# Performance work log

Hardware: AMD Instinct MI355X
Metric: run time of the kernel (lower is better)

Reference implementation:

```python
import jax, jax.numpy as jnp
import numpy as np

DIM_LIST = [8, 8, 8, 8, 8, 8, 8, 8]
RANK_LIST = [1, 64, 64, 64, 64, 64, 64, 64, 1]
ORDER = 4                      # tensor_input_order
PADDED_IN = int(np.prod(DIM_LIST[:ORDER]))   # 4096
NUM_OUT = int(np.prod(DIM_LIST[ORDER:]))     # 4096
BATCH = 8192
NUM_IN = 4000                  # < PADDED_IN, exercises padding path


def setup_inputs() -> dict:
    key = jax.random.key(0)
    keys = jax.random.split(key, 10)
    x = jax.random.normal(keys[0], (BATCH, NUM_IN), dtype=jnp.float32)
    cores = {}
    for i in range(8):
        shp = (RANK_LIST[i], DIM_LIST[i], RANK_LIST[i + 1])
        cores[f"c{i}"] = 0.1 * jax.random.normal(keys[1 + i], shp, dtype=jnp.float32)
    bias = jax.random.normal(keys[9], (NUM_OUT,), dtype=jnp.float32)
    return {"x": x, **cores, "bias": bias}


def _tt_forward(x, cores, bias):
    B = x.shape[0]
    pad = PADDED_IN - x.shape[-1]
    xp = jnp.pad(x, ((0, 0), (0, pad))) if pad > 0 else x
    # ---- contract input modes with first ORDER cores ----
    z = xp.reshape(B, DIM_LIST[0], -1)            # (B, d0, M)
    z = jnp.einsum('bdm,dr->bmr', z, cores[0][0])  # core0 has r0=1
    for i in range(1, ORDER):
        d = DIM_LIST[i]
        Bz, M, r = z.shape
        z = z.reshape(B, d, M // d, r)
        z = jnp.einsum('bdmr,rds->bms', z, cores[i])
    # z: (B, 1, r_k)
    y = z
    # ---- expand output modes with remaining cores ----
    for i in range(ORDER, len(DIM_LIST)):
        y = jnp.einsum('bpr,rds->bpds', y, cores[i])
        y = y.reshape(B, -1, cores[i].shape[-1])
    out = y.reshape(B, -1)[:, :NUM_OUT]
    return out + bias


def reference(x, c0, c1, c2, c3, c4, c5, c6, c7, bias):
    cores = [c0, c1, c2, c3, c4, c5, c6, c7]
    return _tt_forward(x, cores, bias)
```

## Files before the change

### kernel.cpp

```cpp
#include <hip/hip_runtime.h>
#include <hip/hip_bf16.h>


typedef __attribute__((ext_vector_type(8))) short short8;
typedef __attribute__((ext_vector_type(4))) short s16x4;
typedef __attribute__((ext_vector_type(4))) float f32x4;

__device__ __forceinline__ short f2bf(float f) {
    union { float f; unsigned u; } c; c.f = f;
    unsigned u = c.u;
    unsigned r = (u + 0x7fffu + ((u >> 16) & 1u)) >> 16;
    return (short)r;
}

__global__ __launch_bounds__(64) void tt_heads(
    const float* __restrict__ c0, const float* __restrict__ c1,
    const float* __restrict__ c6, const float* __restrict__ c7,
    float* __restrict__ A2, float* __restrict__ B6) {
    const int t = threadIdx.x;
    if (blockIdx.x < 64) {
        const int b = blockIdx.x, i = b >> 3, d = b & 7;
        float acc = 0.f;
        for (int r = 0; r < 64; ++r)
            acc += c0[i * 64 + r] * c1[(r * 8 + d) * 64 + t];
        A2[b * 64 + t] = acc;
    } else {
        const int r = blockIdx.x - 64, d = t >> 3, j = t & 7;
        float acc = 0.f;
        for (int q = 0; q < 64; ++q)
            acc += c6[(r * 8 + d) * 64 + q] * c7[q * 8 + j];
        B6[r * 64 + t] = acc;
    }
}

__global__ __launch_bounds__(64) void tt_seconds(
    const float* __restrict__ A2, const float* __restrict__ c2,
    const float* __restrict__ B6, const float* __restrict__ c5,
    float* __restrict__ A3, float* __restrict__ B5) {
    const int t = threadIdx.x;
    if (blockIdx.x < 512) {
        const int row = blockIdx.x, i = row >> 3, d = row & 7;
        float acc = 0.f;
        for (int r = 0; r < 64; ++r)
            acc += A2[i * 64 + r] * c2[(r * 8 + d) * 64 + t];
        A3[row * 64 + t] = acc;
    } else {
        const int bb = blockIdx.x - 512, r = bb >> 3, d = bb & 7;
        float acc = 0.f;
        for (int q = 0; q < 64; ++q)
            acc += c5[(r * 8 + d) * 64 + q] * B6[q * 64 + t];
        B5[r * 512 + d * 64 + t] = acc;
    }
}

__global__ __launch_bounds__(256) void tt_chain_wide(
    const float* __restrict__ A3, const float* __restrict__ c3,
    const float* __restrict__ B5, const float* __restrict__ c4,
    short* __restrict__ A4t, short* __restrict__ B4t) {
    const int bid = blockIdx.x, t = threadIdx.x;
    if (bid < 1024) {
        const int row = (bid << 2) | (t >> 6);
        const int s = t & 63;
        const int i = row >> 3, d = row & 7;
        float acc = 0.f;
        for (int r = 0; r < 64; ++r)
            acc += A3[i * 64 + r] * c3[(r * 8 + d) * 64 + s];
        A4t[s * 4096 + row] = f2bf(acc);
    } else {
        const int rd = bid - 1024;
        const int r = rd >> 3, d = rd & 7;
        for (int j = t; j < 512; j += 256) {
            float acc = 0.f;
            for (int q = 0; q < 64; ++q)
                acc += c4[(r * 8 + d) * 64 + q] * B5[q * 512 + j];
            B4t[(d * 512 + j) * 64 + r] = f2bf(acc);
        }
    }
}

__global__ __launch_bounds__(1024, 8) void gemm1_v2(
    const float* __restrict__ x, const short* __restrict__ A4t,
    short* __restrict__ zb) {
    __shared__ float zsm[16 * 1024];
    const int tid = threadIdx.x, wave = tid >> 6, lane = tid & 63;
    const int m0 = blockIdx.x << 4;
    const int r16 = lane & 15, hi = lane >> 4, kq = hi << 3;
    const float* xp = x + (long)(m0 + r16) * 4000 + kq;

    f32x4 acc[4] = {};
#pragma unroll 2
    for (int t = wave; t < 125; t += 16) {
        const int k0 = t << 5;
        f32x4 u0 = *(const f32x4*)(xp + k0);
        f32x4 u1 = *(const f32x4*)(xp + k0 + 4);
        short8 a;
        a[0] = f2bf(u0[0]); a[1] = f2bf(u0[1]);
        a[2] = f2bf(u0[2]); a[3] = f2bf(u0[3]);
        a[4] = f2bf(u1[0]); a[5] = f2bf(u1[1]);
        a[6] = f2bf(u1[2]); a[7] = f2bf(u1[3]);
#pragma unroll
        for (int f = 0; f < 4; ++f) {
            short8 b = *(const short8*)(A4t + (f * 16 + r16) * 4096 + k0 + kq);
            acc[f] = __builtin_amdgcn_mfma_f32_16x16x32_bf16(a, b, acc[f], 0, 0, 0);
        }
    }
    const int prow = hi << 2;
#pragma unroll
    for (int f = 0; f < 4; ++f)
#pragma unroll
        for (int u = 0; u < 4; ++u)
            zsm[wave * 1024 + (prow + u) * 64 + f * 16 + r16] = acc[f][u];
    __syncthreads();
    if (tid < 256) {
        const f32x4* zp = (const f32x4*)zsm;
        f32x4 s = zp[tid];
#pragma unroll
        for (int w = 1; w < 16; ++w) s += zp[w * 256 + tid];
        s16x4 o;
#pragma unroll
        for (int u = 0; u < 4; ++u) o[u] = f2bf(s[u]);
        const int orow = tid >> 4, ocol = (tid & 15) << 2;
        *(s16x4*)(zb + (m0 + orow) * 64 + ocol) = o;
    }
}

#define BM 128
#define BN 128
#define BK 32

template <int K>
__global__ __launch_bounds__(256) void gemm_bias_kernel(
    const short* __restrict__ A,
    const short* __restrict__ Bt,
    const float* __restrict__ bias,
    float* __restrict__ C) {
    constexpr int N = 4096;
    __shared__ short As[BM * BK];
    __shared__ short Bs[BN * BK];

    const int tid  = threadIdx.x;
    const int wave = tid >> 6;
    const int lane = tid & 63;

    const int bid = blockIdx.x;
    const int wg  = (bid & 7) * 256 + (bid >> 3);
    const int m0 = (wg >> 5) * BM;
    const int n0 = (wg & 31) * BN;

    const int c0i = tid;
    const int c1i = 256 + tid;
    const short* gA0 = A  + (m0 + (c0i >> 2)) * K + ((c0i & 3) << 3);
    const short* gA1 = A  + (m0 + (c1i >> 2)) * K + ((c1i & 3) << 3);
    const short* gB0 = Bt + (n0 + (c0i >> 2)) * K + ((c0i & 3) << 3);
    const short* gB1 = Bt + (n0 + (c1i >> 2)) * K + ((c1i & 3) << 3);
    short* lA0 = As + wave * 512;
    short* lA1 = As + 2048 + wave * 512;
    short* lB0 = Bs + wave * 512;
    short* lB1 = Bs + 2048 + wave * 512;

    const int wr = (wave >> 1) << 6;
    const int wc = (wave & 1) << 6;
    const int r16 = lane & 15;
    const int kq  = (lane >> 4) << 3;

    f32x4 acc[4][4] = {};

    for (int kt = 0; kt < K / BK; ++kt) {
        __builtin_amdgcn_global_load_lds((const __attribute__((address_space(1))) void*)gA0,
                                         (__attribute__((address_space(3))) void*)lA0, 16, 0, 0);
        __builtin_amdgcn_global_load_lds((const __attribute__((address_space(1))) void*)gA1,
                                         (__attribute__((address_space(3))) void*)lA1, 16, 0, 0);
        __builtin_amdgcn_global_load_lds((const __attribute__((address_space(1))) void*)gB0,
                                         (__attribute__((address_space(3))) void*)lB0, 16, 0, 0);
        __builtin_amdgcn_global_load_lds((const __attribute__((address_space(1))) void*)gB1,
                                         (__attribute__((address_space(3))) void*)lB1, 16, 0, 0);
        gA0 += BK; gA1 += BK; gB0 += BK; gB1 += BK;
        __syncthreads();

        short8 a[4], b[4];
#pragma unroll
        for (int f = 0; f < 4; ++f) {
            a[f] = *(const short8*)(As + (wr + f * 16 + r16) * BK + kq);
            b[f] = *(const short8*)(Bs + (wc + f * 16 + r16) * BK + kq);
        }
#pragma unroll
        for (int i = 0; i < 4; ++i)
#pragma unroll
            for (int j = 0; j < 4; ++j)
                acc[i][j] = __builtin_amdgcn_mfma_f32_16x16x32_bf16(
                    a[i], b[j], acc[i][j], 0, 0, 0);
        __syncthreads();
    }

    const int crow = m0 + wr + ((lane >> 4) << 2);
    const int ccol = n0 + wc + r16;
#pragma unroll
    for (int i = 0; i < 4; ++i) {
#pragma unroll
        for (int j = 0; j < 4; ++j) {
            const int r = crow + i * 16;
            const int c = ccol + j * 16;
            const float bz = bias[c];
#pragma unroll
            for (int u = 0; u < 4; ++u)
                C[(r + u) * N + c] = acc[i][j][u] + bz;
        }
    }
}

extern "C" void kernel_launch(void* const* d_in, const int* in_sizes, int n_in,
                              void* d_out, int out_size, void* d_ws, size_t ws_size,
                              hipStream_t stream) {
    const float* x    = (const float*)d_in[0];
    const float* c0   = (const float*)d_in[1];
    const float* c1   = (const float*)d_in[2];
    const float* c2   = (const float*)d_in[3];
    const float* c3   = (const float*)d_in[4];
    const float* c4   = (const float*)d_in[5];
    const float* c5   = (const float*)d_in[6];
    const float* c6   = (const float*)d_in[7];
    const float* c7   = (const float*)d_in[8];
    const float* bias = (const float*)d_in[9];
    float* out = (float*)d_out;

    char* ws = (char*)d_ws;
    short* zb  = (short*)ws;
    short* A4t = (short*)(ws + (1u << 20));
    short* B4t = (short*)(ws + (1u << 20) + (512u << 10));
    float* A2  = (float*)(ws + (2u << 20));
    float* A3  = A2 + 64 * 64;
    float* B6  = A3 + 512 * 64;
    float* B5  = B6 + 64 * 64;

    tt_heads<<<128, 64, 0, stream>>>(c0, c1, c6, c7, A2, B6);
    tt_seconds<<<1024, 64, 0, stream>>>(A2, c2, B6, c5, A3, B5);
    tt_chain_wide<<<1536, 256, 0, stream>>>(A3, c3, B5, c4, A4t, B4t);

    gemm1_v2<<<512, 1024, 0, stream>>>(x, A4t, zb);
    gemm_bias_kernel<64><<<2048, 256, 0, stream>>>(zb, B4t, bias, out);
}
```

Measured before the change: 96.09 us.

## Store A4 in MFMA fragment order and stage GEMM epilogue through LDS

The A4 factor is now written in a fragment-major layout, so each lane in gemm1 reads its 16-byte B operand from one contiguous 1 KB block per fragment instead of rows strided by 8 KB. The final GEMM's epilogue now goes through shared memory, reusing the operand buffers, so each thread writes full 16-byte float4 rows of the output with the bias added as a vector, replacing scattered scalar stores. This adds extra barriers and LDS traffic in the epilogue, and the producer kernel's writes become more scattered.

Result: faster. 81.62 us (-15.1%).

```diff
diff --git a/kernel.cpp b/kernel.cpp
--- a/kernel.cpp
+++ b/kernel.cpp
@@ -56,16 +56,17 @@
 __global__ __launch_bounds__(256) void tt_chain_wide(
     const float* __restrict__ A3, const float* __restrict__ c3,
     const float* __restrict__ B5, const float* __restrict__ c4,
-    short* __restrict__ A4t, short* __restrict__ B4t) {
+    short* __restrict__ A4f, short* __restrict__ B4t) {
     const int bid = blockIdx.x, t = threadIdx.x;
     if (bid < 1024) {
-        const int row = (bid << 2) | (t >> 6);
+        const int k = (bid << 2) | (t >> 6);
         const int s = t & 63;
-        const int i = row >> 3, d = row & 7;
+        const int i = k >> 3, d = k & 7;
         float acc = 0.f;
         for (int r = 0; r < 64; ++r)
             acc += A3[i * 64 + r] * c3[(r * 8 + d) * 64 + s];
-        A4t[s * 4096 + row] = f2bf(acc);
+        A4f[(((k >> 5) * 4 + (s >> 4)) << 9) + (((k >> 3) & 3) << 7) +
+            ((s & 15) << 3) + (k & 7)] = f2bf(acc);
     } else {
         const int rd = bid - 1024;
         const int r = rd >> 3, d = rd & 7;
@@ -79,13 +80,14 @@
 }
 
 __global__ __launch_bounds__(1024, 8) void gemm1_v2(
-    const float* __restrict__ x, const short* __restrict__ A4t,
+    const float* __restrict__ x, const short* __restrict__ A4f,
     short* __restrict__ zb) {
     __shared__ float zsm[16 * 1024];
     const int tid = threadIdx.x, wave = tid >> 6, lane = tid & 63;
     const int m0 = blockIdx.x << 4;
     const int r16 = lane & 15, hi = lane >> 4, kq = hi << 3;
     const float* xp = x + (long)(m0 + r16) * 4000 + kq;
+    const short* a4p = A4f + (lane << 3);
 
     f32x4 acc[4] = {};
 #pragma unroll 2
@@ -100,7 +102,7 @@
         a[6] = f2bf(u1[2]); a[7] = f2bf(u1[3]);
 #pragma unroll
         for (int f = 0; f < 4; ++f) {
-            short8 b = *(const short8*)(A4t + (f * 16 + r16) * 4096 + k0 + kq);
+            short8 b = *(const short8*)(a4p + (((t << 2) + f) << 9));
             acc[f] = __builtin_amdgcn_mfma_f32_16x16x32_bf16(a, b, acc[f], 0, 0, 0);
         }
     }
@@ -135,8 +137,10 @@
     const float* __restrict__ bias,
     float* __restrict__ C) {
     constexpr int N = 4096;
-    __shared__ short As[BM * BK];
-    __shared__ short Bs[BN * BK];
+    __shared__ __align__(16) char smem[16384];
+    short* As = (short*)smem;
+    short* Bs = (short*)(smem + 8192);
+    float* eps = (float*)smem;
 
     const int tid  = threadIdx.x;
     const int wave = tid >> 6;
@@ -161,7 +165,8 @@
     const int wr = (wave >> 1) << 6;
     const int wc = (wave & 1) << 6;
     const int r16 = lane & 15;
-    const int kq  = (lane >> 4) << 3;
+    const int hi  = lane >> 4;
+    const int kq  = hi << 3;
 
     f32x4 acc[4][4] = {};
 
@@ -192,18 +197,24 @@
         __syncthreads();
     }
 
-    const int crow = m0 + wr + ((lane >> 4) << 2);
-    const int ccol = n0 + wc + r16;
+    float* slab = eps + wave * 1024;
+    const f32x4 bzv = *(const f32x4*)(bias + n0 + wc + (r16 << 2));
 #pragma unroll
     for (int i = 0; i < 4; ++i) {
-#pragma unroll
-        for (int j = 0; j < 4; ++j) {
-            const int r = crow + i * 16;
-            const int c = ccol + j * 16;
-            const float bz = bias[c];
+        __syncthreads();
+#pragma unroll
+        for (int j = 0; j < 4; ++j)
 #pragma unroll
             for (int u = 0; u < 4; ++u)
-                C[(r + u) * N + c] = acc[i][j][u] + bz;
+                slab[((hi << 2) + u) * 64 + j * 16 + r16] = acc[i][j][u];
+        __syncthreads();
+#pragma unroll
+        for (int c = 0; c < 4; ++c) {
+            const int lrow = (c << 2) + hi;
+            f32x4 v = *(const f32x4*)(slab + lrow * 64 + (r16 << 2));
+            v += bzv;
+            const long row = m0 + wr + i * 16 + lrow;
+            *(f32x4*)(C + row * N + n0 + wc + (r16 << 2)) = v;
         }
     }
 }
@@ -225,7 +236,7 @@
 
     char* ws = (char*)d_ws;
     short* zb  = (short*)ws;
-    short* A4t = (short*)(ws + (1u << 20));
+    short* A4f = (short*)(ws + (1u << 20));
     short* B4t = (short*)(ws + (1u << 20) + (512u << 10));
     float* A2  = (float*)(ws + (2u << 20));
     float* A3  = A2 + 64 * 64;
@@ -234,8 +245,8 @@
 
     tt_heads<<<128, 64, 0, stream>>>(c0, c1, c6, c7, A2, B6);
     tt_seconds<<<1024, 64, 0, stream>>>(A2, c2, B6, c5, A3, B5);
-    tt_chain_wide<<<1536, 256, 0, stream>>>(A3, c3, B5, c4, A4t, B4t);
-
-    gemm1_v2<<<512, 1024, 0, stream>>>(x, A4t, zb);
+    tt_chain_wide<<<1536, 256, 0, stream>>>(A3, c3, B5, c4, A4f, B4t);
+
+    gemm1_v2<<<512, 1024, 0, stream>>>(x, A4f, zb);
     gemm_bias_kernel<64><<<2048, 256, 0, stream>>>(zb, B4t, bias, out);
 }
```
